# Optimization experiments

Measured on AMD Instinct MI355X. Metric: run time of the kernel, lower is better.

## Reference

```python
import jax, jax.numpy as jnp
import numpy as np

NUM_SITES = 64
BOND_DIM = 64
PHYS_DIM = 2
BATCH = 8192
INIT_STD = 0.125  # 1/sqrt(bond_dim)
EPS_AMP = 1e-12
EPS_LOG = 1e-30


def setup_inputs() -> dict:
    key = jax.random.key(0)
    k_cfg, k_l, k_b, k_r = jax.random.split(key, 4)
    configurations = jax.random.randint(k_cfg, (BATCH, NUM_SITES), 0, PHYS_DIM, dtype=jnp.int32)
    left = jax.random.normal(k_l, (PHYS_DIM, BOND_DIM), dtype=jnp.float32) * INIT_STD
    bulk = jax.random.normal(k_b, (NUM_SITES - 2, BOND_DIM, PHYS_DIM, BOND_DIM), dtype=jnp.float32) * INIT_STD
    right = jax.random.normal(k_r, (BOND_DIM, PHYS_DIM), dtype=jnp.float32) * INIT_STD
    return {"configurations": configurations, "left": left, "bulk": bulk, "right": right}


def _psi(configurations, left, bulk, right):
    # configurations: [B, S] int; left: [d, D]; bulk: [S-2, D, d, D]; right: [D, d]
    B = configurations.shape[0]
    env0 = left[configurations[:, 0]]  # [B, D]
    cfg_mid = configurations[:, 1:-1].T  # [S-2, B]

    def step(env, xs):
        site_t, idx = xs  # site_t: [D, d, D], idx: [B]
        D = site_t.shape[0]
        # env @ site (contract left bond), then gather the per-sample physical slice
        tmp = (env @ site_t.reshape(D, -1)).reshape(B, PHYS_DIM, D)  # [B, d, D]
        env = jnp.take_along_axis(tmp, idx[:, None, None], axis=1)[:, 0, :]  # [B, D]
        return env, None

    env, _ = jax.lax.scan(step, env0, (bulk, cfg_mid))
    cols = jnp.take(right, configurations[:, -1], axis=1).T  # [B, D]
    return jnp.sum(env * cols, axis=1)  # [B]


def _log_norm(left, bulk, right):
    env0 = left.T @ left  # [D, D]  (real dtype -> conj trivial)

    def step(carry, site_t):
        env, log_scale = carry
        sm = jnp.transpose(site_t, (1, 0, 2))  # [d, D, D]
        env = jnp.einsum('pdi,de,pej->ij', sm, env, sm)  # sum_p A_p^H env A_p
        scale = jnp.maximum(jnp.max(jnp.abs(env)), EPS_LOG)
        return (env / scale, log_scale + jnp.log(scale)), None

    (env, log_scale), _ = jax.lax.scan(step, (env0, jnp.zeros((), left.dtype)), bulk)
    z = jnp.sum(right * (env @ right))
    return jnp.log(jnp.maximum(z, EPS_LOG)) + log_scale


def reference(configurations, left, bulk, right):
    psi = _psi(configurations, left, bulk, right)
    abs_sq = jnp.maximum(psi * psi, EPS_AMP)
    log_z = _log_norm(left, bulk, right)
    nll = -(jnp.log(abs_sq) - log_z)
    return jnp.mean(nll)
```

## Files before the change

kernel.cpp:

```cpp
#include <hip/hip_runtime.h>
#include <math.h>

#define NBULK 62

typedef __attribute__((ext_vector_type(8))) short bf8_t;
typedef __attribute__((ext_vector_type(4))) float f4_t;

#define MFMA16(a, b, c) __builtin_amdgcn_mfma_f32_16x16x32_bf16((a), (b), (c), 0, 0, 0)

__device__ __forceinline__ unsigned short f2bf(float f) {
    unsigned int u = __float_as_uint(f);
    return (unsigned short)((u + 0x7FFFu + ((u >> 16) & 1u)) >> 16);
}
__device__ __forceinline__ float bf2f(unsigned short h) {
    return __uint_as_float(((unsigned int)h) << 16);
}
__device__ __forceinline__ unsigned cvtpk(float lo, float hi) {
    unsigned r;
    asm("v_cvt_pk_bf16_f32 %0, %1, %2" : "=v"(r) : "v"(lo), "v"(hi));
    return r;
}

#define WS_E_OFF   1024
#define WS_B_OFF   6144
#define WS_NFF_OFF 45056
#define WS_NFB_OFF 1060864
#define WS_PFF_OFF 2097152
#define WS_PFB_OFF 2621440


extern "C" __global__ __launch_bounds__(256)
void mps_precompute(const float* __restrict__ bulkG,
                    unsigned short* __restrict__ NFfG,
                    unsigned short* __restrict__ NFbG,
                    unsigned short* __restrict__ PFfG,
                    unsigned short* __restrict__ PFbG,
                    float* __restrict__ wsF)
{
    extern __shared__ char smemP[];
    const int s = blockIdx.x, tid = threadIdx.x;
    if (s < 62) {
        unsigned short* Ff = (unsigned short*)smemP;
        unsigned short* Fb = Ff + 8192;
        if (s == 0 && tid == 0) {
            wsF[0] = 0.f; wsF[1] = 0.f; wsF[2] = 0.f; wsF[3] = 0.f;
        }
        const float4* src = (const float4*)(bulkG + (size_t)s * 8192);
        for (int c = 0; c < 8; ++c) {
            int idx = tid + c * 256;
            float4 v = src[idx];
            int f  = idx * 4;
            int kk = f >> 7;
            int p  = (f >> 6) & 1;
            int j0 = f & 63;
            float vals[4] = {v.x, v.y, v.z, v.w};
            int qf = (kk >> 2) & 3, rf = kk & 3, mf = kk >> 4;
            int ksf = mf >> 1, jjf = (mf & 1) * 4 + rf;
            int tb = kk >> 4, lnb = kk & 15;
            #pragma unroll
            for (int t2 = 0; t2 < 4; ++t2) {
                int j = j0 + t2;
                unsigned short b = f2bf(vals[t2]);
                int tf = j >> 4, lnf = j & 15;
                Ff[((p * 4 + tf) * 2 + ksf) * 512 + (qf * 16 + lnf) * 8 + jjf] = b;
                int qb = (j >> 2) & 3, rb = j & 3, mb = j >> 4;
                int ksb = mb >> 1, jjb = (mb & 1) * 4 + rb;
                Fb[((p * 4 + tb) * 2 + ksb) * 512 + (qb * 16 + lnb) * 8 + jjb] = b;
            }
        }
        __syncthreads();
        const uint4* ff4 = (const uint4*)Ff;
        const uint4* fb4 = (const uint4*)Fb;
        uint4* fg = (uint4*)(NFfG + (size_t)s * 8192);
        uint4* bg = (uint4*)(NFbG + (size_t)s * 8192);
        for (int c = 0; c < 4; ++c) {
            int idx = tid + c * 256;
            fg[idx] = ff4[idx];
            bg[idx] = fb4[idx];
        }
    } else {
        int pb = s - 62;
        bool pf = pb < 15;
        int u  = pf ? pb : pb - 15;
        int sA = pf ? 2 * u     : 60 - 2 * u;
        int sB = pf ? 2 * u + 1 : 61 - 2 * u;
        unsigned short* A16 = (unsigned short*)smemP;
        unsigned short* B16 = A16 + 8192;
        unsigned short* Sc  = (unsigned short*)smemP;
        {
            const float4* sa4 = (const float4*)(bulkG + (size_t)sA * 8192);
            const float4* sb4 = (const float4*)(bulkG + (size_t)sB * 8192);
            for (int c = 0; c < 8; ++c) {
                int i = tid + c * 256;
                float4 va = sa4[i], vb = sb4[i];
                A16[i * 4 + 0] = f2bf(va.x); A16[i * 4 + 1] = f2bf(va.y);
                A16[i * 4 + 2] = f2bf(va.z); A16[i * 4 + 3] = f2bf(va.w);
                B16[i * 4 + 0] = f2bf(vb.x); B16[i * 4 + 1] = f2bf(vb.y);
                B16[i * 4 + 2] = f2bf(vb.z); B16[i * 4 + 3] = f2bf(vb.w);
            }
        }
        __syncthreads();
        const int d = tid >> 2, iBase = (tid & 3) * 16;
        float acc[4][16];
        #pragma unroll
        for (int c = 0; c < 4; ++c)
            #pragma unroll
            for (int ii = 0; ii < 16; ++ii) acc[c][ii] = 0.f;
        for (int e = 0; e < 64; ++e) {
            float a0 = bf2f(A16[d * 128 + e]);
            float a1 = bf2f(A16[d * 128 + 64 + e]);
            const unsigned short* b0p = B16 + e * 128 + iBase;
            const unsigned short* b1p = b0p + 64;
            #pragma unroll
            for (int ii = 0; ii < 16; ++ii) {
                float b0 = bf2f(b0p[ii]), b1 = bf2f(b1p[ii]);
                acc[0][ii] = fmaf(a0, b0, acc[0][ii]);
                acc[1][ii] = fmaf(a0, b1, acc[1][ii]);
                acc[2][ii] = fmaf(a1, b0, acc[2][ii]);
                acc[3][ii] = fmaf(a1, b1, acc[3][ii]);
            }
        }
        __syncthreads();
        #pragma unroll
        for (int c = 0; c < 4; ++c)
            #pragma unroll
            for (int ii = 0; ii < 16; ++ii) {
                int i = iBase + ii;
                unsigned short vbf = f2bf(acc[c][ii]);
                int idx;
                if (pf)
                    idx = c * 4096 + ((i >> 4) * 2 + (d >> 5)) * 512
                        + ((((d >> 2) & 3) * 16 + (i & 15)) << 3)
                        + ((d >> 4) & 1) * 4 + (d & 3);
                else
                    idx = c * 4096 + ((d >> 4) * 2 + (i >> 5)) * 512
                        + ((((i >> 2) & 3) * 16 + (d & 15)) << 3)
                        + ((i >> 4) & 1) * 4 + (i & 3);
                Sc[idx] = vbf;
            }
        __syncthreads();
        uint4* dst = (uint4*)((pf ? (char*)PFfG : (char*)PFbG) + (size_t)u * 32768);
        const uint4* src4 = (const uint4*)Sc;
        for (int c = 0; c < 8; ++c) {
            int i = tid + c * 256;
            dst[i] = src4[i];
        }
    }
}

__device__ __forceinline__ void pfetch(uint4 (&F)[16], const char* tb, int l16)
{
    #pragma unroll
    for (int i = 0; i < 16; ++i)
        F[i] = *(const uint4*)(tb + i * 1024 + l16);
}

__device__ __forceinline__ void pstep(f4_t (&a)[2][4], const uint4 (&F)[16],
                                      const bf8_t (&B)[2])
{
    #pragma unroll
    for (int p = 0; p < 2; ++p)
        #pragma unroll
        for (int mt = 0; mt < 4; ++mt) { f4_t z = {0.f, 0.f, 0.f, 0.f}; a[p][mt] = z; }
    #pragma unroll
    for (int ks = 0; ks < 2; ++ks)
        #pragma unroll
        for (int p = 0; p < 2; ++p)
            #pragma unroll
            for (int mt = 0; mt < 4; ++mt)
                a[p][mt] = MFMA16(*(const bf8_t*)&F[(p * 4 + mt) * 2 + ks], B[ks], a[p][mt]);
}

__device__ __forceinline__ void ppack(bf8_t (&B)[2], const f4_t (&a)[2][4], bool takeB)
{
    #pragma unroll
    for (int ks = 0; ks < 2; ++ks) {
        unsigned w[4];
        #pragma unroll
        for (int d = 0; d < 4; ++d) {
            int mt = 2 * ks + (d >> 1), r = (d & 1) * 2;
            float x0 = takeB ? a[1][mt][r]     : a[0][mt][r];
            float x1 = takeB ? a[1][mt][r + 1] : a[0][mt][r + 1];
            w[d] = cvtpk(x0, x1);
        }
        uint4 u = {w[0], w[1], w[2], w[3]};
        B[ks] = *(const bf8_t*)&u;
    }
}

extern "C" __global__ __launch_bounds__(256, 1)
void mps_main(const int* __restrict__ cfgG, const float* __restrict__ leftG,
              const float* __restrict__ rightG, float* __restrict__ wsF,
              const unsigned short* __restrict__ NFfG,
              const unsigned short* __restrict__ NFbG,
              const unsigned short* __restrict__ PFfG,
              const unsigned short* __restrict__ PFbG)
{
    extern __shared__ char smem[];
    const int tid  = threadIdx.x;
    const int bid  = blockIdx.x;
    const int wv   = tid >> 6;
    const int lane = tid & 63;
    const int ln   = lane & 15, q = lane >> 4;
    const int l16  = lane * 16;

    if (bid >= 2) {
        const char* NF = (const char*)NFfG;
        uint4 Fa[16], Fb[16];
        pfetch(Fa, NF, l16);
        pfetch(Fb, NF + 16384, l16);
        const int s0 = (bid - 2) * 64 + wv * 16;
        unsigned part = 0;
        {
            const int4* crow = (const int4*)(cfgG + (size_t)(s0 + ln) * 64 + q * 16);
            #pragma unroll
            for (int c = 0; c < 4; ++c) {
                int4 v = crow[c];
                part |= (unsigned)(v.x & 1) << (c * 4 + 0);
                part |= (unsigned)(v.y & 1) << (c * 4 + 1);
                part |= (unsigned)(v.z & 1) << (c * 4 + 2);
                part |= (unsigned)(v.w & 1) << (c * 4 + 3);
            }
        }
        unsigned pp   = __shfl_xor(part, 16);
        unsigned comb = (q & 1) ? (pp | (part << 16)) : (part | (pp << 16));
        unsigned selLo = __shfl(comb, ln);
        unsigned selHi = __shfl(comb, ln + 32);

        bf8_t B[2];
        {
            const float* lp = leftG + (selLo & 1u) * 64;
            #pragma unroll
            for (int ks = 0; ks < 2; ++ks) {
                unsigned w[4];
                #pragma unroll
                for (int d = 0; d < 4; ++d) {
                    int k0 = 16 * (2 * ks + (d >> 1)) + 4 * q + 2 * (d & 1);
                    w[d] = (unsigned)f2bf(lp[k0]) | ((unsigned)f2bf(lp[k0 + 1]) << 16);
                }
                uint4 u = {w[0], w[1], w[2], w[3]};
                B[ks] = *(const bf8_t*)&u;
            }
        }
        f4_t a[2][4];
        #define SELBIT(i) ((bool)((((i) < 32) ? (selLo >> (i)) : (selHi >> ((i) - 32))) & 1u))
        for (int t = 0; t < 60; t += 2) {
            pstep(a, Fa, B);
            pfetch(Fa, NF + (size_t)(t + 2) * 16384, l16);
            __builtin_amdgcn_sched_barrier(0);
            ppack(B, a, SELBIT(t + 1));
            pstep(a, Fb, B);
            pfetch(Fb, NF + (size_t)(t + 3) * 16384, l16);
            __builtin_amdgcn_sched_barrier(0);
            ppack(B, a, SELBIT(t + 2));
        }
        pstep(a, Fa, B);
        ppack(B, a, SELBIT(61));
        pstep(a, Fb, B);
        {
            bool tb2 = SELBIT(62);
            int selL = (int)(selHi >> 31) & 1;
            float psum = 0.f;
            #pragma unroll
            for (int mt = 0; mt < 4; ++mt)
                #pragma unroll
                for (int r = 0; r < 4; ++r) {
                    float v = tb2 ? a[1][mt][r] : a[0][mt][r];
                    psum = fmaf(v, rightG[(16 * mt + 4 * q + r) * 2 + selL], psum);
                }
            psum += __shfl_xor(psum, 16);
            psum += __shfl_xor(psum, 32);
            float lp2 = (lane < 16) ? logf(fmaxf(psum * psum, 1e-12f)) : 0.f;
            #pragma unroll
            for (int o = 1; o < 64; o <<= 1) lp2 += __shfl_xor(lp2, o);
            if (lane == 0) atomicAdd(&wsF[0], lp2);
        }
        #undef SELBIT
    } else {
        unsigned short* XsS = (unsigned short*)smem;
        float* wredS = (float*)(XsS + 8192);

        const bool fwd = (bid == 0);
        const char* PF  = fwd ? (const char*)PFfG : (const char*)PFbG;
        const char* SNG = fwd ? ((const char*)NFfG + (size_t)30 * 16384)
                              : ((const char*)NFbG + (size_t)31 * 16384);
        bf8_t A1[4][2];
        {
            float li0[4], li1[4];
            #pragma unroll
            for (int mt = 0; mt < 4; ++mt) {
                int m = mt * 16 + ln;
                li0[mt] = fwd ? leftG[m]      : rightG[m * 2];
                li1[mt] = fwd ? leftG[64 + m] : rightG[m * 2 + 1];
            }
            #pragma unroll
            for (int ks = 0; ks < 2; ++ks) {
                float k0v[8], k1v[8];
                #pragma unroll
                for (int jj = 0; jj < 8; ++jj) {
                    int K = 16 * (2 * ks + (jj >> 2)) + 4 * q + (jj & 3);
                    k0v[jj] = fwd ? leftG[K]      : rightG[K * 2];
                    k1v[jj] = fwd ? leftG[64 + K] : rightG[K * 2 + 1];
                }
                #pragma unroll
                for (int mt = 0; mt < 4; ++mt) {
                    unsigned w[4];
                    #pragma unroll
                    for (int d = 0; d < 4; ++d) {
                        float x0 = li0[mt] * k0v[2 * d]     + li1[mt] * k1v[2 * d];
                        float x1 = li0[mt] * k0v[2 * d + 1] + li1[mt] * k1v[2 * d + 1];
                        w[d] = cvtpk(x0, x1);
                    }
                    uint4 u = {w[0], w[1], w[2], w[3]};
                    A1[mt][ks] = *(const bf8_t*)&u;
                }
            }
        }
        float lsum = 0.f;
        f4_t acc2s[2][4];
        for (int it = 0; it < 16; ++it) {
            __syncthreads();
            if (it > 0) {
                #pragma unroll
                for (int mt = 0; mt < 4; ++mt)
                    #pragma unroll
                    for (int ks = 0; ks < 2; ++ks)
                        A1[mt][ks] = *(const bf8_t*)&XsS[((it & 1) * 8 + mt * 2 + ks) * 512
                                                         + lane * 8];
            }
            const char* base = (it < 15) ? (PF + (size_t)it * 32768) : SNG;
            const int nb = (it < 15) ? 4 : 2;
            float inv = 1.f;
            if (it > 0) {
                const float* wp = wredS + ((it - 1) & 1) * 4;
                float mm = fmaxf(fmaxf(wp[0], wp[1]), fmaxf(wp[2], wp[3]));
                float sc = fmaxf(mm, 1e-30f);
                inv = 1.f / sc;
                lsum += logf(sc);
            }
            #pragma unroll
            for (int p = 0; p < 2; ++p)
                #pragma unroll
                for (int mt = 0; mt < 4; ++mt) {
                    f4_t z = {0.f, 0.f, 0.f, 0.f};
                    acc2s[p][mt] = z;
                }
            #pragma unroll
            for (int c = 0; c < 4; ++c) {
                if (c >= nb) continue;
                const char* br = base + c * 8192;
                bf8_t B1c[2], A2c[4][2];
                #pragma unroll
                for (int ks = 0; ks < 2; ++ks)
                    B1c[ks] = *(const bf8_t*)(br + (wv * 2 + ks) * 1024 + l16);
                #pragma unroll
                for (int mt = 0; mt < 4; ++mt)
                    #pragma unroll
                    for (int ks = 0; ks < 2; ++ks)
                        A2c[mt][ks] = *(const bf8_t*)(br + (mt * 2 + ks) * 1024 + l16);
                f4_t acc1[4];
                #pragma unroll
                for (int mt = 0; mt < 4; ++mt) { f4_t z = {0.f, 0.f, 0.f, 0.f}; acc1[mt] = z; }
                #pragma unroll
                for (int ks = 0; ks < 2; ++ks)
                    #pragma unroll
                    for (int mt = 0; mt < 4; ++mt)
                        acc1[mt] = MFMA16(A1[mt][ks], B1c[ks], acc1[mt]);
                bf8_t B2[2];
                #pragma unroll
                for (int ks = 0; ks < 2; ++ks) {
                    unsigned w[4];
                    #pragma unroll
                    for (int d = 0; d < 4; ++d) {
                        int mt = 2 * ks + (d >> 1), r = (d & 1) * 2;
                        w[d] = cvtpk(acc1[mt][r], acc1[mt][r + 1]);
                    }
                    uint4 u = {w[0], w[1], w[2], w[3]};
                    B2[ks] = *(const bf8_t*)&u;
                }
                #pragma unroll
                for (int ks = 0; ks < 2; ++ks)
                    #pragma unroll
                    for (int mt = 0; mt < 4; ++mt)
                        acc2s[c & 1][mt] = MFMA16(A2c[mt][ks], B2[ks], acc2s[c & 1][mt]);
            }
            float mx = 0.f;
            #pragma unroll
            for (int mt = 0; mt < 4; ++mt)
                #pragma unroll
                for (int r = 0; r < 4; ++r) {
                    float x = (acc2s[0][mt][r] + acc2s[1][mt][r]) * inv;
                    acc2s[0][mt][r] = x;
                    mx = fmaxf(mx, fabsf(x));
                }
            #pragma unroll
            for (int ks = 0; ks < 2; ++ks) {
                unsigned w[4];
                #pragma unroll
                for (int d = 0; d < 4; ++d) {
                    int mt = 2 * ks + (d >> 1), r = (d & 1) * 2;
                    w[d] = cvtpk(acc2s[0][mt][r], acc2s[0][mt][r + 1]);
                }
                uint4 u = {w[0], w[1], w[2], w[3]};
                *(uint4*)&XsS[(((it + 1) & 1) * 8 + wv * 2 + ks) * 512 + lane * 8] = u;
            }
            #pragma unroll
            for (int o = 32; o > 0; o >>= 1) mx = fmaxf(mx, __shfl_xor(mx, o));
            if (lane == 0) wredS[(it & 1) * 4 + wv] = mx;
        }
        float* dst = wsF + (fwd ? WS_E_OFF : WS_B_OFF);
        #pragma unroll
        for (int mt = 0; mt < 4; ++mt)
            #pragma unroll
            for (int r = 0; r < 4; ++r)
                dst[(16 * mt + 4 * q + r) * 64 + wv * 16 + ln] = acc2s[0][mt][r];
        if (tid == 0) wsF[fwd ? 1 : 2] = lsum;
    }
}

extern "C" __global__ void mps_finalize(const float* __restrict__ wsF, float* __restrict__ out)
{
    const int lane = threadIdx.x;
    const float* E  = wsF + WS_E_OFF;
    const float* Bm = wsF + WS_B_OFF;
    float a = 0.f;
    #pragma unroll 8
    for (int j = 0; j < 64; ++j)
        a = fmaf(E[j * 64 + lane], Bm[j * 64 + lane], a);
    #pragma unroll
    for (int off = 32; off > 0; off >>= 1)
        a += __shfl_down(a, off);
    if (lane == 0) {
        const float z = fmaxf(a, 1e-30f);
        const float log_z = logf(z) + wsF[1] + wsF[2];
        out[0] = log_z - wsF[0] * (1.0f / 8192.0f);
    }
}

extern "C" void kernel_launch(void* const* d_in, const int* in_sizes, int n_in,
                              void* d_out, int out_size, void* d_ws, size_t ws_size,
                              hipStream_t stream)
{
    const int*   cfg   = (const int*)d_in[0];
    const float* left  = (const float*)d_in[1];
    const float* bulk  = (const float*)d_in[2];
    const float* right = (const float*)d_in[3];
    float* wsF = (float*)d_ws;
    unsigned short* NFf = (unsigned short*)((char*)d_ws + WS_NFF_OFF);
    unsigned short* NFb = (unsigned short*)((char*)d_ws + WS_NFB_OFF);
    unsigned short* PFf = (unsigned short*)((char*)d_ws + WS_PFF_OFF);
    unsigned short* PFb = (unsigned short*)((char*)d_ws + WS_PFB_OFF);

    mps_precompute<<<dim3(92), dim3(256), 32768, stream>>>(bulk, NFf, NFb, PFf, PFb, wsF);
    mps_main<<<dim3(130), dim3(256), 16416, stream>>>(cfg, left, right, wsF,
                                                      NFf, NFb, PFf, PFb);
    mps_finalize<<<dim3(1), dim3(64), 0, stream>>>(wsF, (float*)d_out);
}
```

Measured before the change: 118.4 us.

## Process two 16-sample groups per wave to reuse fetched site fragments

Each psi wave now carries two independent environment chains (32 samples) through the site chain, so every site-matrix fragment fetched into registers feeds two sets of MFMAs instead of one. The psi grid shrinks from 128 to 64 blocks, halving global/L2 traffic for the site tensors, and the two interleaved chains give the scheduler independent MFMA work to hide dependency latency. In exchange, each wave holds twice the accumulator and B-operand registers, and only 64 of the CUs on the device now get psi blocks, leaving the rest idle.

```diff
diff --git a/kernel.cpp b/kernel.cpp
--- a/kernel.cpp
+++ b/kernel.cpp
@@ -188,6 +188,56 @@
     }
 }
 
+__device__ __forceinline__ void psi_sel(const int* cfgG, int base, int ln, int q,
+                                        unsigned& selLo, unsigned& selHi)
+{
+    unsigned part = 0;
+    const int4* crow = (const int4*)(cfgG + (size_t)(base + ln) * 64 + q * 16);
+    #pragma unroll
+    for (int c = 0; c < 4; ++c) {
+        int4 v = crow[c];
+        part |= (unsigned)(v.x & 1) << (c * 4 + 0);
+        part |= (unsigned)(v.y & 1) << (c * 4 + 1);
+        part |= (unsigned)(v.z & 1) << (c * 4 + 2);
+        part |= (unsigned)(v.w & 1) << (c * 4 + 3);
+    }
+    unsigned pp   = __shfl_xor(part, 16);
+    unsigned comb = (q & 1) ? (pp | (part << 16)) : (part | (pp << 16));
+    selLo = __shfl(comb, ln);
+    selHi = __shfl(comb, ln + 32);
+}
+
+__device__ __forceinline__ void psi_env0(bf8_t (&B)[2], const float* lp, int q)
+{
+    #pragma unroll
+    for (int ks = 0; ks < 2; ++ks) {
+        unsigned w[4];
+        #pragma unroll
+        for (int d = 0; d < 4; ++d) {
+            int k0 = 16 * (2 * ks + (d >> 1)) + 4 * q + 2 * (d & 1);
+            w[d] = (unsigned)f2bf(lp[k0]) | ((unsigned)f2bf(lp[k0 + 1]) << 16);
+        }
+        uint4 u = {w[0], w[1], w[2], w[3]};
+        B[ks] = *(const bf8_t*)&u;
+    }
+}
+
+__device__ __forceinline__ float psi_dot(const f4_t (&a)[2][4], bool tb2,
+                                         const float* rightG, int selL, int q)
+{
+    float psum = 0.f;
+    #pragma unroll
+    for (int mt = 0; mt < 4; ++mt)
+        #pragma unroll
+        for (int r = 0; r < 4; ++r) {
+            float v = tb2 ? a[1][mt][r] : a[0][mt][r];
+            psum = fmaf(v, rightG[(16 * mt + 4 * q + r) * 2 + selL], psum);
+        }
+    psum += __shfl_xor(psum, 16);
+    psum += __shfl_xor(psum, 32);
+    return psum;
+}
+
 extern "C" __global__ __launch_bounds__(256, 1)
 void mps_main(const int* __restrict__ cfgG, const float* __restrict__ leftG,
               const float* __restrict__ rightG, float* __restrict__ wsF,
@@ -209,73 +259,50 @@
         uint4 Fa[16], Fb[16];
         pfetch(Fa, NF, l16);
         pfetch(Fb, NF + 16384, l16);
-        const int s0 = (bid - 2) * 64 + wv * 16;
-        unsigned part = 0;
-        {
-            const int4* crow = (const int4*)(cfgG + (size_t)(s0 + ln) * 64 + q * 16);
-            #pragma unroll
-            for (int c = 0; c < 4; ++c) {
-                int4 v = crow[c];
-                part |= (unsigned)(v.x & 1) << (c * 4 + 0);
-                part |= (unsigned)(v.y & 1) << (c * 4 + 1);
-                part |= (unsigned)(v.z & 1) << (c * 4 + 2);
-                part |= (unsigned)(v.w & 1) << (c * 4 + 3);
-            }
-        }
-        unsigned pp   = __shfl_xor(part, 16);
-        unsigned comb = (q & 1) ? (pp | (part << 16)) : (part | (pp << 16));
-        unsigned selLo = __shfl(comb, ln);
-        unsigned selHi = __shfl(comb, ln + 32);
-
-        bf8_t B[2];
-        {
-            const float* lp = leftG + (selLo & 1u) * 64;
-            #pragma unroll
-            for (int ks = 0; ks < 2; ++ks) {
-                unsigned w[4];
-                #pragma unroll
-                for (int d = 0; d < 4; ++d) {
-                    int k0 = 16 * (2 * ks + (d >> 1)) + 4 * q + 2 * (d & 1);
-                    w[d] = (unsigned)f2bf(lp[k0]) | ((unsigned)f2bf(lp[k0 + 1]) << 16);
-                }
-                uint4 u = {w[0], w[1], w[2], w[3]};
-                B[ks] = *(const bf8_t*)&u;
-            }
-        }
-        f4_t a[2][4];
-        #define SELBIT(i) ((bool)((((i) < 32) ? (selLo >> (i)) : (selHi >> ((i) - 32))) & 1u))
+        const int s0 = (bid - 2) * 128 + wv * 32;
+        unsigned sl0, sh0, sl1, sh1;
+        psi_sel(cfgG, s0,      ln, q, sl0, sh0);
+        psi_sel(cfgG, s0 + 16, ln, q, sl1, sh1);
+
+        bf8_t B0[2], B1[2];
+        psi_env0(B0, leftG + (sl0 & 1u) * 64, q);
+        psi_env0(B1, leftG + (sl1 & 1u) * 64, q);
+
+        f4_t a0[2][4], a1[2][4];
+        #define SB0(i) ((bool)((((i) < 32) ? (sl0 >> (i)) : (sh0 >> ((i) - 32))) & 1u))
+        #define SB1(i) ((bool)((((i) < 32) ? (sl1 >> (i)) : (sh1 >> ((i) - 32))) & 1u))
         for (int t = 0; t < 60; t += 2) {
-            pstep(a, Fa, B);
+            pstep(a0, Fa, B0);
+            pstep(a1, Fa, B1);
             pfetch(Fa, NF + (size_t)(t + 2) * 16384, l16);
             __builtin_amdgcn_sched_barrier(0);
-            ppack(B, a, SELBIT(t + 1));
-            pstep(a, Fb, B);
+            ppack(B0, a0, SB0(t + 1));
+            ppack(B1, a1, SB1(t + 1));
+            pstep(a0, Fb, B0);
+            pstep(a1, Fb, B1);
             pfetch(Fb, NF + (size_t)(t + 3) * 16384, l16);
             __builtin_amdgcn_sched_barrier(0);
-            ppack(B, a, SELBIT(t + 2));
-        }
-        pstep(a, Fa, B);
-        ppack(B, a, SELBIT(61));
-        pstep(a, Fb, B);
+            ppack(B0, a0, SB0(t + 2));
+            ppack(B1, a1, SB1(t + 2));
+        }
+        pstep(a0, Fa, B0);
+        pstep(a1, Fa, B1);
+        ppack(B0, a0, SB0(61));
+        ppack(B1, a1, SB1(61));
+        pstep(a0, Fb, B0);
+        pstep(a1, Fb, B1);
         {
-            bool tb2 = SELBIT(62);
-            int selL = (int)(selHi >> 31) & 1;
-            float psum = 0.f;
-            #pragma unroll
-            for (int mt = 0; mt < 4; ++mt)
-                #pragma unroll
-                for (int r = 0; r < 4; ++r) {
-                    float v = tb2 ? a[1][mt][r] : a[0][mt][r];
-                    psum = fmaf(v, rightG[(16 * mt + 4 * q + r) * 2 + selL], psum);
-                }
-            psum += __shfl_xor(psum, 16);
-            psum += __shfl_xor(psum, 32);
-            float lp2 = (lane < 16) ? logf(fmaxf(psum * psum, 1e-12f)) : 0.f;
+            float p0 = psi_dot(a0, SB0(62), rightG, (int)(sh0 >> 31) & 1, q);
+            float p1 = psi_dot(a1, SB1(62), rightG, (int)(sh1 >> 31) & 1, q);
+            float lp2 = 0.f;
+            if (lane < 16)
+                lp2 = logf(fmaxf(p0 * p0, 1e-12f)) + logf(fmaxf(p1 * p1, 1e-12f));
             #pragma unroll
             for (int o = 1; o < 64; o <<= 1) lp2 += __shfl_xor(lp2, o);
             if (lane == 0) atomicAdd(&wsF[0], lp2);
         }
-        #undef SELBIT
+        #undef SB0
+        #undef SB1
     } else {
         unsigned short* XsS = (unsigned short*)smem;
         float* wredS = (float*)(XsS + 8192);
@@ -452,7 +479,7 @@
     unsigned short* PFb = (unsigned short*)((char*)d_ws + WS_PFB_OFF);
 
     mps_precompute<<<dim3(92), dim3(256), 32768, stream>>>(bulk, NFf, NFb, PFf, PFb, wsF);
-    mps_main<<<dim3(130), dim3(256), 16416, stream>>>(cfg, left, right, wsF,
-                                                      NFf, NFb, PFf, PFb);
+    mps_main<<<dim3(66), dim3(256), 16416, stream>>>(cfg, left, right, wsF,
+                                                     NFf, NFb, PFf, PFb);
     mps_finalize<<<dim3(1), dim3(64), 0, stream>>>(wsF, (float*)d_out);
 }
```

New measurement: 116.3 us. No clear change (-1.7%).
